# Optimization experiments

Hardware: AMD Instinct MI355X
Metric: run time of the kernel (lower is better)

Reference implementation:

```python
import jax, jax.numpy as jnp
import numpy as np

N_DST = 100000


def setup_inputs() -> dict:
    key = jax.random.key(0)
    ks = jax.random.split(key, 12)
    R, Ns, E, Din, H = 3, 100000, 1000000, 128, 64
    return {
        "dst_feat": jax.random.normal(ks[0], (N_DST, Din), jnp.float32),
        "neigh_feats": jax.random.normal(ks[1], (R, Ns, Din), jnp.float32),
        "Wt": jax.random.normal(ks[2], (R + 1, Din, H), jnp.float32) * 0.05,
        "bt": jnp.zeros((R + 1, H), jnp.float32),
        "attn_l": jax.random.normal(ks[3], (R, H), jnp.float32) * 0.1,
        "attn_r": jax.random.normal(ks[4], (R, H), jnp.float32) * 0.1,
        "W1": jax.random.normal(ks[5], (H, 128), jnp.float32) * 0.1,
        "b1": jnp.zeros((128,), jnp.float32),
        "w2": jax.random.normal(ks[6], (128, 1), jnp.float32) * 0.1,
        "src_idx": jax.random.randint(ks[7], (R, E), 0, Ns, jnp.int32),
        "dst_idx": jax.random.randint(ks[8], (R, E), 0, N_DST, jnp.int32),
    }


def _gat_relation(h_src, h_dst, al, ar, src, dst):
    # el/er: per-node attention logits (dot with attn vectors)
    el = h_src @ al  # [Ns]
    er = h_dst @ ar  # [Nd]
    e = jax.nn.leaky_relu(el[src] + er[dst], 0.01)  # [E]
    # edge softmax per destination node (segment softmax)
    m = jax.ops.segment_max(e, dst, num_segments=N_DST)
    a = jnp.exp(e - m[dst])
    s = jax.ops.segment_sum(a, dst, num_segments=N_DST)
    a = a / s[dst]
    # weighted aggregation: sum_e a_e * h_src[src_e]
    out = jax.ops.segment_sum(h_src[src] * a[:, None], dst, num_segments=N_DST)
    return jax.nn.elu(out)


def reference(dst_feat, neigh_feats, Wt, bt, attn_l, attn_r, W1, b1, w2, src_idx, dst_idx):
    R = neigh_feats.shape[0]
    h_dst = dst_feat @ Wt[0] + bt[0]  # weight_T[0]
    z_r = []
    for r in range(R):
        h_src = neigh_feats[r] @ Wt[r + 1] + bt[r + 1]
        z_r.append(_gat_relation(h_src, h_dst, attn_l[r], attn_r[r], src_idx[r], dst_idx[r]))
    z_r = jnp.stack(z_r, axis=1)  # [N, R, D]
    # semantic attention
    w = (jnp.tanh(z_r @ W1 + b1) @ w2).mean(axis=0)  # [R, 1]
    a_w = jax.nn.softmax(w, axis=0)  # softmax over relations
    z = (z_r * a_w[None]).sum(axis=1)  # [N, D]
    return z
```

## Files before the change

kernel.cpp:

```cpp
#include <hip/hip_runtime.h>
#include <hip/hip_fp16.h>

#define N_DST 100000
#define DIN 128
#define HDIM 64
#define RREL 3
#define NE 1000000

#define NBKT_REL 196
#define NBKT (RREL * NBKT_REL)
#define NSEG (RREL * N_DST)
#define EDGE_CHUNK 16384
#define NBLK_BIN ((RREL * NE + EDGE_CHUNK - 1) / EDGE_CHUNK)

typedef _Float16 f16x8 __attribute__((ext_vector_type(8)));
typedef float f32x4 __attribute__((ext_vector_type(4)));

__global__ __launch_bounds__(256) void k_wprep(const float* __restrict__ Wt,
                                               __half* __restrict__ W16) {
  int g = blockIdx.x * 256 + threadIdx.x;
  int col = g & 63;
  int kb = (g >> 6) & 15;
  int mat = g >> 10;
  const float* wp = Wt + ((size_t)mat * DIN + kb * 8) * HDIM + col;
  f16x8 hv;
#pragma unroll
  for (int j = 0; j < 8; j++) hv[j] = (_Float16)wp[(size_t)j * HDIM];
  *(f16x8*)((unsigned char*)W16 + mat * 16384 + col * 256 + ((kb * 16) ^ ((col & 7) << 4))) = hv;
}

__global__ __launch_bounds__(256) void k_gemm(
    const float* __restrict__ dst_feat, const float* __restrict__ neigh,
    const __half* __restrict__ W16, const float* __restrict__ bt,
    const float* __restrict__ attn_l, const float* __restrict__ attn_r,
    __half* __restrict__ h16, float* __restrict__ el, float* __restrict__ er) {
  const int RB = (N_DST + 127) / 128;
  int mat = blockIdx.x / RB;
  int row0 = (blockIdx.x % RB) * 128;
  const float* A = (mat == 0) ? dst_feat : (neigh + (size_t)(mat - 1) * N_DST * DIN);
  const float* b = bt + mat * HDIM;

  __shared__ __align__(16) unsigned char ldsW[16384];
  int tid = threadIdx.x;

  {
    const float4* wsrc = (const float4*)((const unsigned char*)W16 + (size_t)mat * 16384);
#pragma unroll
    for (int i = 0; i < 4; i++)
      *(float4*)(ldsW + (tid + 256 * i) * 16) = wsrc[tid + 256 * i];
  }

  int w = tid >> 6;
  int l = tid & 63;
  int li = l & 15;
  int hi = l >> 4;

  int r0 = row0 + w * 32 + li;
  int ra = min(r0, N_DST - 1);
  int rb = min(r0 + 16, N_DST - 1);
  const float* pa = A + (size_t)ra * DIN + hi * 8;
  const float* pb = A + (size_t)rb * DIN + hi * 8;

  auto cvt8 = [](const float4& v0, const float4& v1) {
    f16x8 h;
    h[0] = (_Float16)v0.x; h[1] = (_Float16)v0.y;
    h[2] = (_Float16)v0.z; h[3] = (_Float16)v0.w;
    h[4] = (_Float16)v1.x; h[5] = (_Float16)v1.y;
    h[6] = (_Float16)v1.z; h[7] = (_Float16)v1.w;
    return h;
  };

  float4 sa0[2], sb0[2], sa1[2], sb1[2];
  sa0[0] = *(const float4*)(pa);      sa0[1] = *(const float4*)(pa + 4);
  sb0[0] = *(const float4*)(pb);      sb0[1] = *(const float4*)(pb + 4);
  sa1[0] = *(const float4*)(pa + 32); sa1[1] = *(const float4*)(pa + 36);
  sb1[0] = *(const float4*)(pb + 32); sb1[1] = *(const float4*)(pb + 36);

  __syncthreads();

  f32x4 acc[2][4] = {};
#define KS_STEP(KS, SA, SB, PREF_OFF, DO_PREF)                                  \
  {                                                                             \
    f16x8 afa = cvt8(SA[0], SA[1]);                                             \
    f16x8 afb = cvt8(SB[0], SB[1]);                                             \
    if (DO_PREF) {                                                              \
      SA[0] = *(const float4*)(pa + PREF_OFF);                                  \
      SA[1] = *(const float4*)(pa + PREF_OFF + 4);                              \
      SB[0] = *(const float4*)(pb + PREF_OFF);                                  \
      SB[1] = *(const float4*)(pb + PREF_OFF + 4);                              \
    }                                                                           \
    int kbyte = (KS)*64 + hi * 16;                                              \
    _Pragma("unroll") for (int ct = 0; ct < 4; ct++) {                          \
      int col = ct * 16 + li;                                                   \
      f16x8 bf = *(f16x8*)(ldsW + col * 256 + (kbyte ^ ((col & 7) << 4)));      \
      acc[0][ct] = __builtin_amdgcn_mfma_f32_16x16x32_f16(afa, bf, acc[0][ct], 0, 0, 0); \
      acc[1][ct] = __builtin_amdgcn_mfma_f32_16x16x32_f16(afb, bf, acc[1][ct], 0, 0, 0); \
    }                                                                           \
  }
  KS_STEP(0, sa0, sb0, 64, 1)
  KS_STEP(1, sa1, sb1, 96, 1)
  KS_STEP(2, sa0, sb0, 0, 0)
  KS_STEP(3, sa1, sb1, 0, 0)
#undef KS_STEP

  float bv[4];
#pragma unroll
  for (int ct = 0; ct < 4; ct++) bv[ct] = b[ct * 16 + li];
#pragma unroll
  for (int rt = 0; rt < 2; rt++)
#pragma unroll
    for (int ct = 0; ct < 4; ct++)
#pragma unroll
      for (int j = 0; j < 4; j++) acc[rt][ct][j] += bv[ct];

  if (mat == 0) {
#pragma unroll
    for (int r = 0; r < RREL; r++) {
      float av[4];
#pragma unroll
      for (int ct = 0; ct < 4; ct++) av[ct] = attn_r[r * HDIM + ct * 16 + li];
#pragma unroll
      for (int rt = 0; rt < 2; rt++) {
        float p[4];
#pragma unroll
        for (int j = 0; j < 4; j++)
          p[j] = acc[rt][0][j] * av[0] + acc[rt][1][j] * av[1] +
                 acc[rt][2][j] * av[2] + acc[rt][3][j] * av[3];
#pragma unroll
        for (int o = 1; o < 16; o <<= 1)
#pragma unroll
          for (int j = 0; j < 4; j++) p[j] += __shfl_xor(p[j], o);
        if (li == 0) {
#pragma unroll
          for (int j = 0; j < 4; j++) {
            int gr = row0 + w * 32 + rt * 16 + hi * 4 + j;
            if (gr < N_DST) er[r * N_DST + gr] = p[j];
          }
        }
      }
    }
  } else {
    int r = mat - 1;
    float av[4];
#pragma unroll
    for (int ct = 0; ct < 4; ct++) av[ct] = attn_l[r * HDIM + ct * 16 + li];
#pragma unroll
    for (int rt = 0; rt < 2; rt++) {
      float p[4];
#pragma unroll
      for (int j = 0; j < 4; j++)
        p[j] = acc[rt][0][j] * av[0] + acc[rt][1][j] * av[1] +
               acc[rt][2][j] * av[2] + acc[rt][3][j] * av[3];
#pragma unroll
      for (int o = 1; o < 16; o <<= 1)
#pragma unroll
        for (int j = 0; j < 4; j++) p[j] += __shfl_xor(p[j], o);
      if (li == 0) {
#pragma unroll
        for (int j = 0; j < 4; j++) {
          int gr = row0 + w * 32 + rt * 16 + hi * 4 + j;
          if (gr < N_DST) el[r * N_DST + gr] = p[j];
        }
      }
    }
    __half* hb = h16 + (size_t)r * N_DST * HDIM;
#pragma unroll
    for (int rt = 0; rt < 2; rt++)
#pragma unroll
      for (int j = 0; j < 4; j++) {
        int gr = row0 + w * 32 + rt * 16 + hi * 4 + j;
        if (gr < N_DST) {
#pragma unroll
          for (int ct = 0; ct < 4; ct++)
            hb[(size_t)gr * HDIM + ct * 16 + li] = __float2half(acc[rt][ct][j]);
        }
      }
  }
}


__global__ __launch_bounds__(256) void k_hist(const int* __restrict__ dst_idx,
                                              int* __restrict__ hist) {
  __shared__ int h[NBKT];
  int tid = threadIdx.x;
  int blk = blockIdx.x;
  for (int i = tid; i < NBKT; i += 256) h[i] = 0;
  __syncthreads();
  int e0 = blk * EDGE_CHUNK;
  int e1 = min(e0 + EDGE_CHUNK, RREL * NE);
  for (int idx = e0 + tid; idx < e1; idx += 256) {
    int r = idx / NE;
    int d = dst_idx[idx];
    atomicAdd(&h[r * NBKT_REL + (d >> 9)], 1);
  }
  __syncthreads();
  for (int i = tid; i < NBKT; i += 256)
    hist[(size_t)i * NBLK_BIN + blk] = h[i];
}

__global__ __launch_bounds__(256) void k_colscan(int* __restrict__ hist,
                                                 int* __restrict__ bcounts) {
  __shared__ int sm[256];
  int b = blockIdx.x;
  int tid = threadIdx.x;
  int v = (tid < NBLK_BIN) ? hist[(size_t)b * NBLK_BIN + tid] : 0;
  sm[tid] = v;
  __syncthreads();
  for (int off = 1; off < 256; off <<= 1) {
    int t = (tid >= off) ? sm[tid - off] : 0;
    __syncthreads();
    sm[tid] += t;
    __syncthreads();
  }
  if (tid < NBLK_BIN) hist[(size_t)b * NBLK_BIN + tid] = sm[tid] - v;
  if (tid == 255) bcounts[b] = sm[255];
}

__global__ __launch_bounds__(256) void k_bscan(const int* __restrict__ bcounts,
                                               int* __restrict__ bucket_base,
                                               int* __restrict__ offsets) {
  __shared__ int sm[256];
  int tid = threadIdx.x;
  int base = tid * 3;
  int c[3];
#pragma unroll
  for (int k = 0; k < 3; k++) c[k] = (base + k < NBKT) ? bcounts[base + k] : 0;
  int tsum = c[0] + c[1] + c[2];
  sm[tid] = tsum;
  __syncthreads();
  for (int off = 1; off < 256; off <<= 1) {
    int v = (tid >= off) ? sm[tid - off] : 0;
    __syncthreads();
    sm[tid] += v;
    __syncthreads();
  }
  int run = sm[tid] - tsum;
#pragma unroll
  for (int k = 0; k < 3; k++) {
    if (base + k < NBKT) bucket_base[base + k] = run;
    run += c[k];
  }
  if (tid == 255) bucket_base[NBKT] = sm[255];
  if (tid == 0) offsets[NSEG] = RREL * NE;
}

__global__ __launch_bounds__(256) void k_place(const int* __restrict__ src_idx,
                                               const int* __restrict__ dst_idx,
                                               const int* __restrict__ hist,
                                               const int* __restrict__ bucket_base,
                                               unsigned* __restrict__ tmp) {
  __shared__ int cur[NBKT];
  int tid = threadIdx.x;
  int blk = blockIdx.x;
  for (int i = tid; i < NBKT; i += 256)
    cur[i] = bucket_base[i] + hist[(size_t)i * NBLK_BIN + blk];
  __syncthreads();
  int e0 = blk * EDGE_CHUNK;
  int e1 = min(e0 + EDGE_CHUNK, RREL * NE);
  for (int idx = e0 + tid; idx < e1; idx += 256) {
    int r = idx / NE;
    int d = dst_idx[idx];
    int s = src_idx[idx];
    int bucket = r * NBKT_REL + (d >> 9);
    int pos = atomicAdd(&cur[bucket], 1);
    tmp[pos] = ((unsigned)(d & 511) << 17) | (unsigned)s;
  }
}

__global__ __launch_bounds__(256) void k_bucket_csr(
    const int* __restrict__ bucket_base, const unsigned* __restrict__ tmp,
    int* __restrict__ src_sorted, int* __restrict__ offsets) {
  __shared__ int cnt[512];
  __shared__ int base_l[512];
  __shared__ int sm[256];
  int b = blockIdx.x;
  int r = b / NBKT_REL;
  int brel = b - r * NBKT_REL;
  int gbase = bucket_base[b];
  int gend = bucket_base[b + 1];
  int tid = threadIdx.x;
  cnt[tid] = 0;
  cnt[tid + 256] = 0;
  __syncthreads();
  for (int e = gbase + tid; e < gend; e += 256)
    atomicAdd(&cnt[tmp[e] >> 17], 1);
  __syncthreads();
  int c0 = cnt[2 * tid], c1 = cnt[2 * tid + 1];
  int tsum = c0 + c1;
  sm[tid] = tsum;
  __syncthreads();
  for (int off = 1; off < 256; off <<= 1) {
    int v = (tid >= off) ? sm[tid - off] : 0;
    __syncthreads();
    sm[tid] += v;
    __syncthreads();
  }
  int run = sm[tid] - tsum;
  base_l[2 * tid] = run;
  base_l[2 * tid + 1] = run + c0;
  __syncthreads();
  for (int s = tid; s < 512; s += 256) {
    int dst = (brel << 9) + s;
    if (dst < N_DST) offsets[r * N_DST + dst] = gbase + base_l[s];
    cnt[s] = 0;
  }
  __syncthreads();
  for (int e = gbase + tid; e < gend; e += 256) {
    unsigned w = tmp[e];
    int s = w >> 17;
    int pos = gbase + base_l[s] + atomicAdd(&cnt[s], 1);
    src_sorted[pos] = (int)(w & 0x1FFFFu);
  }
}

__global__ __launch_bounds__(256) void k_aggregate(
    const int* __restrict__ offsets, const int* __restrict__ src_sorted,
    const float* __restrict__ el, const float* __restrict__ er,
    const __half* __restrict__ h16, float* __restrict__ zbuf) {
  int gw = blockIdx.x * 32 + (threadIdx.x >> 3);
  int li = threadIdx.x & 7;
  if (gw >= NSEG) return;
  int r = gw / N_DST;
  int start = offsets[gw], end = offsets[gw + 1];
  float erv = er[gw];
  const unsigned char* hs = (const unsigned char*)(h16 + (size_t)r * N_DST * HDIM);
  const float* elr = el + (size_t)r * N_DST;
  float acc[8] = {};
  float ssum = 0.f;
  int sNext = (start < end) ? src_sorted[start] : 0;
  for (int e = start; e < end; ++e) {
    int s = sNext;
    if (e + 1 < end) sNext = src_sorted[e + 1];
    float x = elr[s] + erv;
    float4 rv = *(const float4*)(hs + (unsigned)(s * 128 + li * 16));
    x = (x > 0.f) ? x : 0.01f * x;
    float a = __expf(x);
    ssum += a;
    const __half2* hp = (const __half2*)&rv;
#pragma unroll
    for (int q = 0; q < 4; q++) {
      float2 f = __half22float2(hp[q]);
      acc[2 * q] += a * f.x;
      acc[2 * q + 1] += a * f.y;
    }
  }
  float inv = (end > start) ? 1.f / ssum : 0.f;
  float zv[8];
#pragma unroll
  for (int q = 0; q < 8; q++) {
    float v = acc[q] * inv;
    zv[q] = (v > 0.f) ? v : (__expf(v) - 1.f);
  }
  float* zp = zbuf + (size_t)gw * HDIM + li * 8;
  *(float4*)zp = make_float4(zv[0], zv[1], zv[2], zv[3]);
  *(float4*)(zp + 4) = make_float4(zv[4], zv[5], zv[6], zv[7]);
}

__global__ __launch_bounds__(256) void k_semantic(
    const float* __restrict__ zbuf, const float* __restrict__ W1,
    const float* __restrict__ b1, const float* __restrict__ w2,
    float* __restrict__ w_acc) {
  __shared__ __align__(16) unsigned char lds[32 * 1024];
  unsigned char* ldsZ = lds;
  unsigned char* ldsW = lds + 16384;
  __shared__ float wsum[RREL];
  int tid = threadIdx.x;
  if (tid < RREL) wsum[tid] = 0.f;
  int row0 = blockIdx.x * 128;

  {
    int col = tid & 127;
    int kq = tid >> 7;
    const float* wp = W1 + (size_t)(kq * 32) * 128 + col;
    float wr[32];
#pragma unroll
    for (int m = 0; m < 32; m++) wr[m] = wp[(size_t)m * 128];
#pragma unroll
    for (int m8 = 0; m8 < 4; m8++) {
      f16x8 hv;
#pragma unroll
      for (int j = 0; j < 8; j++) hv[j] = (_Float16)wr[m8 * 8 + j];
      int byt = kq * 64 + m8 * 16;
      *(f16x8*)(ldsW + col * 128 + (byt ^ ((col & 7) << 4))) = hv;
    }
  }
#pragma unroll
  for (int i = 0; i < 4; i++) {
    int s = tid + 256 * i;
    int row = s >> 3;
    int kb = s & 7;
    int gr = row0 + row;
    if (gr >= NSEG) gr = NSEG - 1;
    const float* zp = zbuf + (size_t)gr * HDIM + kb * 8;
    float4 v0 = *(const float4*)zp;
    float4 v1 = *(const float4*)(zp + 4);
    f16x8 hv;
    hv[0] = (_Float16)v0.x; hv[1] = (_Float16)v0.y;
    hv[2] = (_Float16)v0.z; hv[3] = (_Float16)v0.w;
    hv[4] = (_Float16)v1.x; hv[5] = (_Float16)v1.y;
    hv[6] = (_Float16)v1.z; hv[7] = (_Float16)v1.w;
    *(f16x8*)(ldsZ + row * 128 + ((kb * 16) ^ ((row & 7) << 4))) = hv;
  }
  __syncthreads();

  int w = tid >> 6;
  int l = tid & 63;
  int li = l & 15;
  int hi = l >> 4;
  f32x4 acc[2][8] = {};
#pragma unroll
  for (int ks = 0; ks < 2; ks++) {
    int kbyte = ks * 64 + hi * 16;
    f16x8 af[2], bf[8];
#pragma unroll
    for (int rt = 0; rt < 2; rt++) {
      int row = w * 32 + rt * 16 + li;
      af[rt] = *(f16x8*)(ldsZ + row * 128 + (kbyte ^ ((row & 7) << 4)));
    }
#pragma unroll
    for (int ct = 0; ct < 8; ct++) {
      int col = ct * 16 + li;
      bf[ct] = *(f16x8*)(ldsW + col * 128 + (kbyte ^ ((col & 7) << 4)));
    }
#pragma unroll
    for (int rt = 0; rt < 2; rt++)
#pragma unroll
      for (int ct = 0; ct < 8; ct++)
        acc[rt][ct] = __builtin_amdgcn_mfma_f32_16x16x32_f16(af[rt], bf[ct], acc[rt][ct], 0, 0, 0);
  }

  float p[2][4] = {};
#pragma unroll
  for (int ct = 0; ct < 8; ct++) {
    float b1v = b1[ct * 16 + li];
    float w2v = w2[ct * 16 + li];
#pragma unroll
    for (int rt = 0; rt < 2; rt++)
#pragma unroll
      for (int j = 0; j < 4; j++) {
        float x = acc[rt][ct][j] + b1v;
        float ex = __expf(2.f * x);
        p[rt][j] += (1.f - 2.f / (ex + 1.f)) * w2v;
      }
  }
#pragma unroll
  for (int o = 1; o < 16; o <<= 1)
#pragma unroll
    for (int rt = 0; rt < 2; rt++)
#pragma unroll
      for (int j = 0; j < 4; j++) p[rt][j] += __shfl_xor(p[rt][j], o);
  if (li == 0) {
#pragma unroll
    for (int rt = 0; rt < 2; rt++)
#pragma unroll
      for (int j = 0; j < 4; j++) {
        int row = row0 + w * 32 + rt * 16 + hi * 4 + j;
        if (row < NSEG) atomicAdd(&wsum[row / N_DST], p[rt][j]);
      }
  }
  __syncthreads();
  if (tid < RREL) atomicAdd(&w_acc[tid], wsum[tid]);
}

__global__ __launch_bounds__(256) void k_final(const float* __restrict__ zbuf,
                                               const float* __restrict__ w_acc,
                                               float* __restrict__ out) {
  int idx = blockIdx.x * 256 + threadIdx.x;
  if (idx >= N_DST * HDIM / 4) return;
  const float invN = 1.0f / N_DST;
  float w0 = w_acc[0] * invN, w1 = w_acc[1] * invN, w2v = w_acc[2] * invN;
  float m = fmaxf(w0, fmaxf(w1, w2v));
  float e0 = __expf(w0 - m), e1 = __expf(w1 - m), e2 = __expf(w2v - m);
  float inv = 1.f / (e0 + e1 + e2);
  e0 *= inv; e1 *= inv; e2 *= inv;
  size_t o = (size_t)idx * 4;
  const size_t stride = (size_t)N_DST * HDIM;
  float4 z0 = *(const float4*)(zbuf + o);
  float4 z1 = *(const float4*)(zbuf + stride + o);
  float4 z2 = *(const float4*)(zbuf + 2 * stride + o);
  float4 r;
  r.x = e0 * z0.x + e1 * z1.x + e2 * z2.x;
  r.y = e0 * z0.y + e1 * z1.y + e2 * z2.y;
  r.z = e0 * z0.z + e1 * z1.z + e2 * z2.z;
  r.w = e0 * z0.w + e1 * z1.w + e2 * z2.w;
  *(float4*)(out + o) = r;
}

extern "C" void kernel_launch(void* const* d_in, const int* in_sizes, int n_in,
                              void* d_out, int out_size, void* d_ws, size_t ws_size,
                              hipStream_t stream) {
  const float* dst_feat = (const float*)d_in[0];
  const float* neigh = (const float*)d_in[1];
  const float* Wt = (const float*)d_in[2];
  const float* bt = (const float*)d_in[3];
  const float* attn_l = (const float*)d_in[4];
  const float* attn_r = (const float*)d_in[5];
  const float* W1 = (const float*)d_in[6];
  const float* b1 = (const float*)d_in[7];
  const float* w2 = (const float*)d_in[8];
  const int* src_idx = (const int*)d_in[9];
  const int* dst_idx = (const int*)d_in[10];
  float* out = (float*)d_out;

  char* p = (char*)d_ws;
  auto alloc = [&](size_t bytes) {
    char* q = p;
    p += (bytes + 255) & ~(size_t)255;
    return (void*)q;
  };
  __half* h16 = (__half*)alloc((size_t)RREL * N_DST * HDIM * 2);
  __half* W16 = (__half*)alloc((size_t)(RREL + 1) * HDIM * DIN * 2);
  float* el = (float*)alloc((size_t)RREL * N_DST * 4);
  float* er = (float*)alloc((size_t)RREL * N_DST * 4);
  float* zbuf = (float*)alloc((size_t)RREL * N_DST * HDIM * 4);
  float* w_acc = (float*)alloc(64);
  int* offsets = (int*)alloc(((size_t)NSEG + 1) * 4);
  int* hist = (int*)alloc((size_t)NBKT * NBLK_BIN * 4);
  int* bcounts = (int*)alloc((size_t)NBKT * 4);
  int* bucket_base = (int*)alloc((size_t)(NBKT + 1) * 4);
  unsigned* tmp = (unsigned*)alloc((size_t)RREL * NE * 4);
  int* src_sorted = (int*)alloc((size_t)RREL * NE * 4);

  hipMemsetAsync(w_acc, 0, 64, stream);

  k_wprep<<<16, 256, 0, stream>>>(Wt, W16);
  k_gemm<<<4 * ((N_DST + 127) / 128), 256, 0, stream>>>(dst_feat, neigh, W16, bt, attn_l, attn_r,
                                                        h16, el, er);
  k_hist<<<NBLK_BIN, 256, 0, stream>>>(dst_idx, hist);
  k_colscan<<<NBKT, 256, 0, stream>>>(hist, bcounts);
  k_bscan<<<1, 256, 0, stream>>>(bcounts, bucket_base, offsets);
  k_place<<<NBLK_BIN, 256, 0, stream>>>(src_idx, dst_idx, hist, bucket_base, tmp);
  k_bucket_csr<<<NBKT, 256, 0, stream>>>(bucket_base, tmp, src_sorted, offsets);
  k_aggregate<<<(NSEG + 31) / 32, 256, 0, stream>>>(offsets, src_sorted, el, er, h16, zbuf);
  k_semantic<<<(NSEG + 127) / 128, 256, 0, stream>>>(zbuf, W1, b1, w2, w_acc);
  k_final<<<(N_DST * HDIM / 4 + 255) / 256, 256, 0, stream>>>(zbuf, w_acc, out);
}
```

Baseline: 511.8 us.

## Make feature GEMM persistent with prefetch; permute h16 columns for vector stores

```diff
diff --git a/kernel.cpp b/kernel.cpp
--- a/kernel.cpp
+++ b/kernel.cpp
@@ -15,6 +15,7 @@
 
 typedef _Float16 f16x8 __attribute__((ext_vector_type(8)));
 typedef float f32x4 __attribute__((ext_vector_type(4)));
+
 
 __global__ __launch_bounds__(256) void k_wprep(const float* __restrict__ Wt,
                                                __half* __restrict__ W16) {
@@ -35,31 +36,38 @@
     const float* __restrict__ attn_l, const float* __restrict__ attn_r,
     __half* __restrict__ h16, float* __restrict__ el, float* __restrict__ er) {
   const int RB = (N_DST + 127) / 128;
-  int mat = blockIdx.x / RB;
-  int row0 = (blockIdx.x % RB) * 128;
+  int mat = blockIdx.x & 3;
+  int bslot = blockIdx.x >> 2;
   const float* A = (mat == 0) ? dst_feat : (neigh + (size_t)(mat - 1) * N_DST * DIN);
   const float* b = bt + mat * HDIM;
 
   __shared__ __align__(16) unsigned char ldsW[16384];
   int tid = threadIdx.x;
-
   {
     const float4* wsrc = (const float4*)((const unsigned char*)W16 + (size_t)mat * 16384);
 #pragma unroll
     for (int i = 0; i < 4; i++)
       *(float4*)(ldsW + (tid + 256 * i) * 16) = wsrc[tid + 256 * i];
   }
-
   int w = tid >> 6;
   int l = tid & 63;
   int li = l & 15;
   int hi = l >> 4;
 
-  int r0 = row0 + w * 32 + li;
-  int ra = min(r0, N_DST - 1);
-  int rb = min(r0 + 16, N_DST - 1);
-  const float* pa = A + (size_t)ra * DIN + hi * 8;
-  const float* pb = A + (size_t)rb * DIN + hi * 8;
+  float bv[4], av0[4], av1[4], av2[4];
+#pragma unroll
+  for (int ct = 0; ct < 4; ct++) bv[ct] = b[ct * 16 + li];
+  if (mat == 0) {
+#pragma unroll
+    for (int ct = 0; ct < 4; ct++) {
+      av0[ct] = attn_r[0 * HDIM + ct * 16 + li];
+      av1[ct] = attn_r[1 * HDIM + ct * 16 + li];
+      av2[ct] = attn_r[2 * HDIM + ct * 16 + li];
+    }
+  } else {
+#pragma unroll
+    for (int ct = 0; ct < 4; ct++) av0[ct] = attn_l[(mat - 1) * HDIM + ct * 16 + li];
+  }
 
   auto cvt8 = [](const float4& v0, const float4& v1) {
     f16x8 h;
@@ -70,112 +78,117 @@
     return h;
   };
 
-  float4 sa0[2], sb0[2], sa1[2], sb1[2];
-  sa0[0] = *(const float4*)(pa);      sa0[1] = *(const float4*)(pa + 4);
-  sb0[0] = *(const float4*)(pb);      sb0[1] = *(const float4*)(pb + 4);
-  sa1[0] = *(const float4*)(pa + 32); sa1[1] = *(const float4*)(pa + 36);
-  sb1[0] = *(const float4*)(pb + 32); sb1[1] = *(const float4*)(pb + 36);
-
-  __syncthreads();
-
-  f32x4 acc[2][4] = {};
-#define KS_STEP(KS, SA, SB, PREF_OFF, DO_PREF)                                  \
-  {                                                                             \
-    f16x8 afa = cvt8(SA[0], SA[1]);                                             \
-    f16x8 afb = cvt8(SB[0], SB[1]);                                             \
-    if (DO_PREF) {                                                              \
-      SA[0] = *(const float4*)(pa + PREF_OFF);                                  \
-      SA[1] = *(const float4*)(pa + PREF_OFF + 4);                              \
-      SB[0] = *(const float4*)(pb + PREF_OFF);                                  \
-      SB[1] = *(const float4*)(pb + PREF_OFF + 4);                              \
-    }                                                                           \
-    int kbyte = (KS)*64 + hi * 16;                                              \
-    _Pragma("unroll") for (int ct = 0; ct < 4; ct++) {                          \
-      int col = ct * 16 + li;                                                   \
-      f16x8 bf = *(f16x8*)(ldsW + col * 256 + (kbyte ^ ((col & 7) << 4)));      \
-      acc[0][ct] = __builtin_amdgcn_mfma_f32_16x16x32_f16(afa, bf, acc[0][ct], 0, 0, 0); \
-      acc[1][ct] = __builtin_amdgcn_mfma_f32_16x16x32_f16(afb, bf, acc[1][ct], 0, 0, 0); \
-    }                                                                           \
-  }
-  KS_STEP(0, sa0, sb0, 64, 1)
-  KS_STEP(1, sa1, sb1, 96, 1)
-  KS_STEP(2, sa0, sb0, 0, 0)
-  KS_STEP(3, sa1, sb1, 0, 0)
-#undef KS_STEP
-
-  float bv[4];
-#pragma unroll
-  for (int ct = 0; ct < 4; ct++) bv[ct] = b[ct * 16 + li];
-#pragma unroll
-  for (int rt = 0; rt < 2; rt++)
-#pragma unroll
-    for (int ct = 0; ct < 4; ct++)
-#pragma unroll
-      for (int j = 0; j < 4; j++) acc[rt][ct][j] += bv[ct];
-
-  if (mat == 0) {
-#pragma unroll
-    for (int r = 0; r < RREL; r++) {
-      float av[4];
-#pragma unroll
-      for (int ct = 0; ct < 4; ct++) av[ct] = attn_r[r * HDIM + ct * 16 + li];
-#pragma unroll
-      for (int rt = 0; rt < 2; rt++) {
-        float p[4];
-#pragma unroll
-        for (int j = 0; j < 4; j++)
-          p[j] = acc[rt][0][j] * av[0] + acc[rt][1][j] * av[1] +
-                 acc[rt][2][j] * av[2] + acc[rt][3][j] * av[3];
-#pragma unroll
-        for (int o = 1; o < 16; o <<= 1)
-#pragma unroll
-          for (int j = 0; j < 4; j++) p[j] += __shfl_xor(p[j], o);
-        if (li == 0) {
-#pragma unroll
-          for (int j = 0; j < 4; j++) {
-            int gr = row0 + w * 32 + rt * 16 + hi * 4 + j;
-            if (gr < N_DST) er[r * N_DST + gr] = p[j];
+#define APTR(T, OFS) (A + (size_t)min((T) * 128 + w * 32 + li + (OFS), N_DST - 1) * DIN + hi * 8)
+
+#define LOADH(P, PA, PB, H)                       \
+  do {                                            \
+    P[0] = *(const float4*)((PA) + (H) * 64);     \
+    P[1] = *(const float4*)((PA) + (H) * 64 + 4); \
+    P[2] = *(const float4*)((PB) + (H) * 64);     \
+    P[3] = *(const float4*)((PB) + (H) * 64 + 4); \
+    P[4] = *(const float4*)((PA) + (H) * 64 + 32);\
+    P[5] = *(const float4*)((PA) + (H) * 64 + 36);\
+    P[6] = *(const float4*)((PB) + (H) * 64 + 32);\
+    P[7] = *(const float4*)((PB) + (H) * 64 + 36);\
+  } while (0)
+
+#define COMPH(P, H)                                                                        \
+  do {                                                                                     \
+    f16x8 fa0 = cvt8(P[0], P[1]);                                                          \
+    f16x8 fb0 = cvt8(P[2], P[3]);                                                          \
+    int kb0 = (2 * (H)) * 64 + hi * 16;                                                    \
+    _Pragma("unroll") for (int ct = 0; ct < 4; ct++) {                                     \
+      int col = ct * 16 + li;                                                              \
+      f16x8 bf = *(f16x8*)(ldsW + col * 256 + (kb0 ^ ((col & 7) << 4)));                   \
+      acc[0][ct] = __builtin_amdgcn_mfma_f32_16x16x32_f16(fa0, bf, acc[0][ct], 0, 0, 0);   \
+      acc[1][ct] = __builtin_amdgcn_mfma_f32_16x16x32_f16(fb0, bf, acc[1][ct], 0, 0, 0);   \
+    }                                                                                      \
+    f16x8 fa1 = cvt8(P[4], P[5]);                                                          \
+    f16x8 fb1 = cvt8(P[6], P[7]);                                                          \
+    int kb1 = (2 * (H) + 1) * 64 + hi * 16;                                                \
+    _Pragma("unroll") for (int ct = 0; ct < 4; ct++) {                                     \
+      int col = ct * 16 + li;                                                              \
+      f16x8 bf = *(f16x8*)(ldsW + col * 256 + (kb1 ^ ((col & 7) << 4)));                   \
+      acc[0][ct] = __builtin_amdgcn_mfma_f32_16x16x32_f16(fa1, bf, acc[0][ct], 0, 0, 0);   \
+      acc[1][ct] = __builtin_amdgcn_mfma_f32_16x16x32_f16(fb1, bf, acc[1][ct], 0, 0, 0);   \
+    }                                                                                      \
+  } while (0)
+
+#define RELRED(AV, DST)                                                                \
+  do {                                                                                 \
+    _Pragma("unroll") for (int rt = 0; rt < 2; rt++) {                                 \
+      float p[4];                                                                      \
+      _Pragma("unroll") for (int j = 0; j < 4; j++)                                    \
+          p[j] = acc[rt][0][j] * AV[0] + acc[rt][1][j] * AV[1] +                        \
+                 acc[rt][2][j] * AV[2] + acc[rt][3][j] * AV[3];                         \
+      _Pragma("unroll") for (int o = 1; o < 16; o <<= 1)                               \
+        _Pragma("unroll") for (int j = 0; j < 4; j++) p[j] += __shfl_xor(p[j], o);     \
+      if (li == 0) {                                                                   \
+        _Pragma("unroll") for (int j = 0; j < 4; j++) {                                \
+          int gr = trow + rt * 16 + hi * 4 + j;                                        \
+          if (gr < N_DST) (DST)[gr] = p[j];                                            \
+        }                                                                              \
+      }                                                                                \
+    }                                                                                  \
+  } while (0)
+
+  float4 P0[8], P1[8];
+  int t = bslot;
+  const float* pa = APTR(t, 0);
+  const float* pb = APTR(t, 16);
+  LOADH(P0, pa, pb, 0);
+  __syncthreads();
+
+  for (;;) {
+    LOADH(P1, pa, pb, 1);
+    f32x4 acc[2][4] = {};
+    COMPH(P0, 0);
+    int tn = t + 192;
+    bool more = tn < RB;
+    const float* pan = pa;
+    const float* pbn = pb;
+    if (more) {
+      pan = APTR(tn, 0);
+      pbn = APTR(tn, 16);
+      LOADH(P0, pan, pbn, 0);
+    }
+    COMPH(P1, 1);
+
+    int trow = t * 128 + w * 32;
+#pragma unroll
+    for (int rt = 0; rt < 2; rt++)
+#pragma unroll
+      for (int ct = 0; ct < 4; ct++)
+#pragma unroll
+        for (int j = 0; j < 4; j++) acc[rt][ct][j] += bv[ct];
+
+    if (mat == 0) {
+      RELRED(av0, er + 0 * N_DST);
+      RELRED(av1, er + 1 * N_DST);
+      RELRED(av2, er + 2 * N_DST);
+    } else {
+      RELRED(av0, el + (size_t)(mat - 1) * N_DST);
+      __half* hb = h16 + (size_t)(mat - 1) * N_DST * HDIM;
+#pragma unroll
+      for (int rt = 0; rt < 2; rt++)
+#pragma unroll
+        for (int j = 0; j < 4; j++) {
+          int gr = trow + rt * 16 + hi * 4 + j;
+          if (gr < N_DST) {
+            union { __half2 h2[2]; float2 f2; } u;
+            u.h2[0] = __floats2half2_rn(acc[rt][0][j], acc[rt][1][j]);
+            u.h2[1] = __floats2half2_rn(acc[rt][2][j], acc[rt][3][j]);
+            *(float2*)(hb + (size_t)gr * HDIM + li * 4) = u.f2;
           }
         }
-      }
-    }
-  } else {
-    int r = mat - 1;
-    float av[4];
-#pragma unroll
-    for (int ct = 0; ct < 4; ct++) av[ct] = attn_l[r * HDIM + ct * 16 + li];
-#pragma unroll
-    for (int rt = 0; rt < 2; rt++) {
-      float p[4];
-#pragma unroll
-      for (int j = 0; j < 4; j++)
-        p[j] = acc[rt][0][j] * av[0] + acc[rt][1][j] * av[1] +
-               acc[rt][2][j] * av[2] + acc[rt][3][j] * av[3];
-#pragma unroll
-      for (int o = 1; o < 16; o <<= 1)
-#pragma unroll
-        for (int j = 0; j < 4; j++) p[j] += __shfl_xor(p[j], o);
-      if (li == 0) {
-#pragma unroll
-        for (int j = 0; j < 4; j++) {
-          int gr = row0 + w * 32 + rt * 16 + hi * 4 + j;
-          if (gr < N_DST) el[r * N_DST + gr] = p[j];
-        }
-      }
-    }
-    __half* hb = h16 + (size_t)r * N_DST * HDIM;
-#pragma unroll
-    for (int rt = 0; rt < 2; rt++)
-#pragma unroll
-      for (int j = 0; j < 4; j++) {
-        int gr = row0 + w * 32 + rt * 16 + hi * 4 + j;
-        if (gr < N_DST) {
-#pragma unroll
-          for (int ct = 0; ct < 4; ct++)
-            hb[(size_t)gr * HDIM + ct * 16 + li] = __float2half(acc[rt][ct][j]);
-        }
-      }
-  }
+    }
+    if (!more) break;
+    t = tn; pa = pan; pb = pbn;
+  }
+#undef APTR
+#undef LOADH
+#undef COMPH
+#undef RELRED
 }
 
 
@@ -371,10 +384,13 @@
   {
     int col = tid & 127;
     int kq = tid >> 7;
-    const float* wp = W1 + (size_t)(kq * 32) * 128 + col;
     float wr[32];
 #pragma unroll
-    for (int m = 0; m < 32; m++) wr[m] = wp[(size_t)m * 128];
+    for (int m = 0; m < 32; m++) {
+      int k = kq * 32 + m;
+      int srck = (k & 3) * 16 + (k >> 2);
+      wr[m] = W1[(size_t)srck * 128 + col];
+    }
 #pragma unroll
     for (int m8 = 0; m8 < 4; m8++) {
       f16x8 hv;
@@ -465,25 +481,48 @@
 __global__ __launch_bounds__(256) void k_final(const float* __restrict__ zbuf,
                                                const float* __restrict__ w_acc,
                                                float* __restrict__ out) {
-  int idx = blockIdx.x * 256 + threadIdx.x;
-  if (idx >= N_DST * HDIM / 4) return;
+  __shared__ float c[64][68];
+  int tid = threadIdx.x;
+  int n0 = blockIdx.x * 64;
   const float invN = 1.0f / N_DST;
   float w0 = w_acc[0] * invN, w1 = w_acc[1] * invN, w2v = w_acc[2] * invN;
   float m = fmaxf(w0, fmaxf(w1, w2v));
   float e0 = __expf(w0 - m), e1 = __expf(w1 - m), e2 = __expf(w2v - m);
   float inv = 1.f / (e0 + e1 + e2);
   e0 *= inv; e1 *= inv; e2 *= inv;
-  size_t o = (size_t)idx * 4;
   const size_t stride = (size_t)N_DST * HDIM;
-  float4 z0 = *(const float4*)(zbuf + o);
-  float4 z1 = *(const float4*)(zbuf + stride + o);
-  float4 z2 = *(const float4*)(zbuf + 2 * stride + o);
-  float4 r;
-  r.x = e0 * z0.x + e1 * z1.x + e2 * z2.x;
-  r.y = e0 * z0.y + e1 * z1.y + e2 * z2.y;
-  r.z = e0 * z0.z + e1 * z1.z + e2 * z2.z;
-  r.w = e0 * z0.w + e1 * z1.w + e2 * z2.w;
-  *(float4*)(out + o) = r;
+#pragma unroll
+  for (int i = 0; i < 4; i++) {
+    int idx = tid + 256 * i;
+    int nl = idx >> 4;
+    int q = idx & 15;
+    int n = n0 + nl;
+    float4 rv = make_float4(0.f, 0.f, 0.f, 0.f);
+    if (n < N_DST) {
+      size_t o = (size_t)n * HDIM + q * 4;
+      float4 z0 = *(const float4*)(zbuf + o);
+      float4 z1 = *(const float4*)(zbuf + stride + o);
+      float4 z2 = *(const float4*)(zbuf + 2 * stride + o);
+      rv.x = e0 * z0.x + e1 * z1.x + e2 * z2.x;
+      rv.y = e0 * z0.y + e1 * z1.y + e2 * z2.y;
+      rv.z = e0 * z0.z + e1 * z1.z + e2 * z2.z;
+      rv.w = e0 * z0.w + e1 * z1.w + e2 * z2.w;
+    }
+    *(float4*)(&c[nl][q * 4]) = rv;
+  }
+  __syncthreads();
+  int nl = tid >> 2;
+  int dq = tid & 3;
+  int n = n0 + nl;
+  if (n < N_DST) {
+    float o16[16];
+#pragma unroll
+    for (int i = 0; i < 16; i++) o16[i] = c[nl][i * 4 + dq];
+    float4* op = (float4*)(out + (size_t)n * HDIM + dq * 16);
+#pragma unroll
+    for (int qq = 0; qq < 4; qq++)
+      op[qq] = make_float4(o16[qq * 4], o16[qq * 4 + 1], o16[qq * 4 + 2], o16[qq * 4 + 3]);
+  }
 }
 
 extern "C" void kernel_launch(void* const* d_in, const int* in_sizes, int n_in,
@@ -524,8 +563,7 @@
   hipMemsetAsync(w_acc, 0, 64, stream);
 
   k_wprep<<<16, 256, 0, stream>>>(Wt, W16);
-  k_gemm<<<4 * ((N_DST + 127) / 128), 256, 0, stream>>>(dst_feat, neigh, W16, bt, attn_l, attn_r,
-                                                        h16, el, er);
+  k_gemm<<<768, 256, 0, stream>>>(dst_feat, neigh, W16, bt, attn_l, attn_r, h16, el, er);
   k_hist<<<NBLK_BIN, 256, 0, stream>>>(dst_idx, hist);
   k_colscan<<<NBKT, 256, 0, stream>>>(hist, bcounts);
   k_bscan<<<1, 256, 0, stream>>>(bcounts, bucket_base, offsets);
@@ -533,5 +571,5 @@
   k_bucket_csr<<<NBKT, 256, 0, stream>>>(bucket_base, tmp, src_sorted, offsets);
   k_aggregate<<<(NSEG + 31) / 32, 256, 0, stream>>>(offsets, src_sorted, el, er, h16, zbuf);
   k_semantic<<<(NSEG + 127) / 128, 256, 0, stream>>>(zbuf, W1, b1, w2, w_acc);
-  k_final<<<(N_DST * HDIM / 4 + 255) / 256, 256, 0, stream>>>(zbuf, w_acc, out);
-}
+  k_final<<<(N_DST + 63) / 64, 256, 0, stream>>>(zbuf, w_acc, out);
+}
```

Measured after the change: 523.3 us. 1.02x slower.
